# Kernel optimization log

Hardware: AMD Instinct MI355X
Metric: run time of the kernel (lower is better)

The kernel has to match this reference:

```python
import jax, jax.numpy as jnp
import numpy as np

S = 3000    # number of candidate spans (rows of g_i)
P = 80000   # total (mention, antecedent) pairs
GI = 768    # gi_dim
DD = 20     # distance/genre/speaker embedding dim
HID = 150   # mlp hidden dim (fixed in source)
ORDER = 2   # N: one higher-order refinement pass


def setup_inputs() -> dict:
    key = jax.random.key(0)
    ks = jax.random.split(key, 18)
    gij = 3 * GI + 3 * DD
    g_i = jax.random.normal(ks[0], (S, GI), jnp.float32)
    mention_scores = jax.random.normal(ks[1], (S, 1), jnp.float32)
    # sorted segment ids: ragged antecedent counts per mention, grouped contiguously
    mention_ids = jnp.sort(jax.random.randint(ks[2], (P,), 0, S, dtype=jnp.int32))
    antecedent_ids = jax.random.randint(ks[3], (P,), 0, S, dtype=jnp.int32)
    dist_bins = jax.random.randint(ks[4], (P,), 0, 10, dtype=jnp.int32)
    genre_ids = jax.random.randint(ks[5], (P,), 0, 7, dtype=jnp.int32) + 1   # 1..7, 0 is padding_idx
    speaker_ids = jax.random.randint(ks[6], (P,), 0, 2, dtype=jnp.int32) + 1  # 1..2, 0 is padding_idx
    w = lambda k, shp: 0.02 * jax.random.normal(k, shp, jnp.float32)
    dist_emb = w(ks[7], (10, DD))
    genre_emb = w(ks[8], (8, DD)).at[0].set(0.0)     # padding_idx=0
    speaker_emb = w(ks[9], (3, DD)).at[0].set(0.0)   # padding_idx=0
    W1 = w(ks[10], (gij, HID)); b1 = jnp.zeros((HID,), jnp.float32)
    W2 = w(ks[11], (HID, HID)); b2 = jnp.zeros((HID,), jnp.float32)
    W3 = w(ks[12], (HID, 1)); b3 = jnp.zeros((1,), jnp.float32)
    Wf = w(ks[13], (2 * GI, 1)); bf = jnp.zeros((1,), jnp.float32)
    return {"g_i": g_i, "mention_scores": mention_scores, "mention_ids": mention_ids,
            "antecedent_ids": antecedent_ids, "dist_bins": dist_bins, "genre_ids": genre_ids,
            "speaker_ids": speaker_ids, "dist_emb": dist_emb, "genre_emb": genre_emb,
            "speaker_emb": speaker_emb, "W1": W1, "b1": b1, "W2": W2, "b2": b2,
            "W3": W3, "b3": b3, "Wf": Wf, "bf": bf}


def _mlp(x, W1, b1, W2, b2, W3, b3):
    h = jax.nn.relu(x @ W1 + b1)
    h = jax.nn.relu(h @ W2 + b2)
    return h @ W3 + b3


def reference(g_i, mention_scores, mention_ids, antecedent_ids, dist_bins, genre_ids,
              speaker_ids, dist_emb, genre_emb, speaker_emb, W1, b1, W2, b2, W3, b3, Wf, bf):
    phi = jnp.concatenate([dist_emb[dist_bins], genre_emb[genre_ids], speaker_emb[speaker_ids]], axis=1)  # [P,60]
    seg = dict(num_segments=S, indices_are_sorted=True)
    g = g_i
    scores = None
    for n in range(ORDER):
        i_g = g[mention_ids]                # [P,GI] gather
        j_g = g[antecedent_ids]             # [P,GI] gather
        pairs = jnp.concatenate([i_g, j_g, i_g * j_g, phi], axis=1)  # [P,gij]
        scores = _mlp(pairs, W1, b1, W2, b2, W3, b3)                 # [P,1]
        if n < ORDER - 1:
            # higher_order_refinement: ragged segment softmax + weighted scatter update
            s = scores[:, 0]
            seg_max = jax.ops.segment_max(s, mention_ids, **seg)
            safe_max = jnp.where(jnp.isfinite(seg_max), seg_max, 0.0)
            e = jnp.exp(s - safe_max[mention_ids])
            denom = jax.ops.segment_sum(e, mention_ids, **seg)
            attn = e / jnp.where(denom > 0, denom, 1.0)[mention_ids]
            weighted = jax.ops.segment_sum(attn[:, None] * j_g, mention_ids, **seg)  # [S,GI]
            counts = jax.ops.segment_sum(jnp.ones_like(s), mention_ids, **seg)
            f = jax.nn.sigmoid(jnp.concatenate([g, weighted], axis=1) @ Wf + bf)  # [S,1]
            # NOTE: faithful to the source bug: f * mention_id (the integer index), not f * mention_g
            ids_f = jnp.arange(S, dtype=g.dtype)[:, None]
            g_new = f * ids_f + (1.0 - f) * weighted
            g = jnp.where(counts[:, None] > 0, g_new, g)
    s_i = mention_scores[mention_ids]
    s_j = mention_scores[antecedent_ids]
    coref_scores = s_i + s_j + scores       # [P,1]
    # segment softmax with an extra epsilon (score 0) logit per mention
    c = coref_scores[:, 0]
    seg_max = jax.ops.segment_max(c, mention_ids, **seg)
    m = jnp.maximum(jnp.where(jnp.isfinite(seg_max), seg_max, 0.0), 0.0)  # include epsilon logit 0
    e = jnp.exp(c - m[mention_ids])
    denom = jax.ops.segment_sum(e, mention_ids, **seg) + jnp.exp(-m)
    pair_probs = e / denom[mention_ids]     # [P]
    eps_probs = jnp.exp(-m) / denom         # [S]
    return coref_scores, pair_probs, eps_probs
```

## Files before the change

kernel.cpp:

```cpp
#include <hip/hip_runtime.h>

#define GI   768
#define HID  150
#define HPAD 160
#define DDIM 20

typedef __attribute__((ext_vector_type(8))) short v8s;
typedef __attribute__((ext_vector_type(16))) float f32x16;

#define MFMA(A, B, C) __builtin_amdgcn_mfma_f32_32x32x16_bf16(A, B, C, 0, 0, 0)

__device__ __forceinline__ ushort bf16rn(float x) {
  unsigned u = __float_as_uint(x);
  return (ushort)((u + 0x7fffu + ((u >> 16) & 1u)) >> 16);
}
__device__ __forceinline__ void bsplit(float x, ushort& h, ushort& l) {
  h = bf16rn(x);
  float fh = __uint_as_float((unsigned)h << 16);
  l = bf16rn(x - fh);
}
__device__ __forceinline__ void tsplit(float x, ushort& h, ushort& l) {
  unsigned u = __float_as_uint(x);
  h = (ushort)(u >> 16);
  float d = x - __uint_as_float(u & 0xffff0000u);
  l = (ushort)(__float_as_uint(d) >> 16);
}
__device__ __forceinline__ uint4 pack8(const ushort* v) {
  uint4 r;
  r.x = v[0] | ((unsigned)v[1] << 16); r.y = v[2] | ((unsigned)v[3] << 16);
  r.z = v[4] | ((unsigned)v[5] << 16); r.w = v[6] | ((unsigned)v[7] << 16);
  return r;
}
__device__ __forceinline__ v8s mk8(const ushort* v) {
  union { uint4 u; v8s s; } t;
  t.u = pack8(v);
  return t.s;
}

__device__ __forceinline__ int qoffb(int row, int kb) {
  return row * 96 + (kb ^ (((row >> 2) & 3) << 4));
}

__global__ void seg_kernel(const int* __restrict__ mI, int* __restrict__ segs,
                           int P, int S) {
  int m = blockIdx.x * 256 + threadIdx.x;
  if (m > S) return;
  int lo = 0, hi = P;
  while (lo < hi) { int mid = (lo + hi) >> 1; if (mI[mid] < m) lo = mid + 1; else hi = mid; }
  segs[m] = lo;
}

__global__ void phi_kernel(const float* __restrict__ de, const float* __restrict__ ge,
                           const float* __restrict__ se, const float* __restrict__ W1,
                           float* __restrict__ phiW) {
  int idx = blockIdx.x * 256 + threadIdx.x;
  if (idx >= 21 * HPAD) return;
  int row = idx / HPAD, h = idx % HPAD;
  float v = 0.f;
  if (h < HID) {
    const float* emb; int off;
    if (row < 10)      { emb = de + row * DDIM;        off = 0; }
    else if (row < 18) { emb = ge + (row - 10) * DDIM; off = DDIM; }
    else               { emb = se + (row - 18) * DDIM; off = 2 * DDIM; }
    for (int k = 0; k < DDIM; ++k) v += emb[k] * W1[(3 * GI + off + k) * HID + h];
  }
  phiW[row * HPAD + h] = v;
}

__global__ void pad2_kernel(const float* __restrict__ W1, const float* __restrict__ W2,
                            const float* __restrict__ b1, const float* __restrict__ b2,
                            const float* __restrict__ W3,
                            ushort* __restrict__ WThi, ushort* __restrict__ WTlo,
                            ushort* __restrict__ WBhi, ushort* __restrict__ WBlo,
                            ushort* __restrict__ W2Bhi, ushort* __restrict__ W2Blo,
                            float* __restrict__ b1p, float2* __restrict__ b2w3) {
  int idx = blockIdx.x * 256 + threadIdx.x;
  if (idx < 480 * GI) {
    int c = idx / GI, r = idx % GI;
    int seg = c / HPAD, h = c % HPAD;
    float x = (h < HID) ? W1[(size_t)(seg * GI + r) * HID + h] : 0.f;
    ushort hh, ll; bsplit(x, hh, ll);
    WThi[idx] = hh; WTlo[idx] = ll; return;
  }
  idx -= 480 * GI;
  if (idx < 5 * 48 * 512) {
    int c = idx / (48 * 512); int r1 = idx % (48 * 512);
    int s = r1 / 512; int r2 = r1 % 512;
    int l = r2 / 8, j = r2 % 8;
    int h = c * 32 + (l & 31);
    int k = s * 16 + 8 * (l >> 5) + j;
    float x = (h < HID) ? W1[(size_t)(2 * GI + k) * HID + h] : 0.f;
    ushort hh, ll; bsplit(x, hh, ll);
    WBhi[idx] = hh; WBlo[idx] = ll; return;
  }
  idx -= 5 * 48 * 512;
  if (idx < 5 * 10 * 512) {
    int rt = idx / (10 * 512); int r1 = idx % (10 * 512);
    int s = r1 / 512; int r2 = r1 % 512;
    int l = r2 / 8, j = r2 % 8;
    int h2 = rt * 32 + (l & 31);
    int k = s * 16 + 8 * (l >> 5) + j;
    float x = (k < HID && h2 < HID) ? W2[(size_t)k * HID + h2] : 0.f;
    ushort hh, ll; bsplit(x, hh, ll);
    W2Bhi[idx] = hh; W2Blo[idx] = ll; return;
  }
  idx -= 5 * 10 * 512;
  if (idx < HPAD) { b1p[idx] = (idx < HID) ? b1[idx] : 0.f; return; }
  idx -= HPAD;
  if (idx < HPAD) {
    b2w3[idx] = make_float2((idx < HID) ? b2[idx] : 0.f, (idx < HID) ? W3[idx] : 0.f);
    return;
  }
}

__global__ __launch_bounds__(320, 4) void pre2_kernel(
    const float* __restrict__ g, const ushort* __restrict__ WThi,
    const ushort* __restrict__ WTlo, float* __restrict__ pre, int S) {
  __shared__ char pool[24576];
  const int t = threadIdx.x;
  const int lane = t & 63, w = t >> 6;
  const int lcol = lane & 31, half = lane >> 5;
  const int row0 = blockIdx.x * 64;
  const int hb = blockIdx.y * HPAD;

  f32x16 acc0 = {}, acc1 = {};
  const ushort* wh = WThi + (size_t)(hb + w * 32 + lcol) * GI + 8 * half;
  const ushort* wl = WTlo + (size_t)(hb + w * 32 + lcol) * GI + 8 * half;

  const int qr = (t < 256) ? (t >> 2) : 0;
  const int qob = qoffb(qr, (t & 3) * 16);
  int srow = row0 + qr; if (srow >= S) srow = S - 1;
  const float* gp = g + (size_t)srow * GI + (t & 3) * 8;

  if (t < 256) {
    float4 a0 = *(const float4*)(gp), a1 = *(const float4*)(gp + 4);
    float xr[8] = {a0.x, a0.y, a0.z, a0.w, a1.x, a1.y, a1.z, a1.w};
    ushort hs[8], ls[8];
#pragma unroll
    for (int j = 0; j < 8; ++j) bsplit(xr[j], hs[j], ls[j]);
    *(uint4*)(pool + qob) = pack8(hs);
    *(uint4*)(pool + 6144 + qob) = pack8(ls);
  }
  v8s cwh0 = *(const v8s*)(wh), cwh1 = *(const v8s*)(wh + 16);
  v8s cwl0 = *(const v8s*)(wl), cwl1 = *(const v8s*)(wl + 16);
  __syncthreads();

  int cur = 0;
#pragma unroll 1
  for (int d0 = 0; d0 < GI; d0 += 32) {
    const bool has = (d0 + 32) < GI;
    const int dn = has ? d0 + 32 : 0;
    float4 na0, na1;
    if (t < 256) { na0 = *(const float4*)(gp + dn); na1 = *(const float4*)(gp + dn + 4); }
    v8s nwh0 = *(const v8s*)(wh + dn), nwh1 = *(const v8s*)(wh + dn + 16);
    v8s nwl0 = *(const v8s*)(wl + dn), nwl1 = *(const v8s*)(wl + dn + 16);

    const char* qh = pool + cur * 12288;
    const char* ql = qh + 6144;
    {
      const int kb = 16 * half;
      v8s a0h = *(const v8s*)(qh + qoffb(lcol, kb));
      v8s a0l = *(const v8s*)(ql + qoffb(lcol, kb));
      acc0 = MFMA(a0h, cwh0, acc0); acc0 = MFMA(a0l, cwh0, acc0); acc0 = MFMA(a0h, cwl0, acc0);
      v8s a1h = *(const v8s*)(qh + qoffb(32 + lcol, kb));
      v8s a1l = *(const v8s*)(ql + qoffb(32 + lcol, kb));
      acc1 = MFMA(a1h, cwh0, acc1); acc1 = MFMA(a1l, cwh0, acc1); acc1 = MFMA(a1h, cwl0, acc1);
    }
    {
      const int kb = 32 + 16 * half;
      v8s a0h = *(const v8s*)(qh + qoffb(lcol, kb));
      v8s a0l = *(const v8s*)(ql + qoffb(lcol, kb));
      acc0 = MFMA(a0h, cwh1, acc0); acc0 = MFMA(a0l, cwh1, acc0); acc0 = MFMA(a0h, cwl1, acc0);
      v8s a1h = *(const v8s*)(qh + qoffb(32 + lcol, kb));
      v8s a1l = *(const v8s*)(ql + qoffb(32 + lcol, kb));
      acc1 = MFMA(a1h, cwh1, acc1); acc1 = MFMA(a1l, cwh1, acc1); acc1 = MFMA(a1h, cwl1, acc1);
    }
    if (has && t < 256) {
      float xr[8] = {na0.x, na0.y, na0.z, na0.w, na1.x, na1.y, na1.z, na1.w};
      ushort hs[8], ls[8];
#pragma unroll
      for (int j = 0; j < 8; ++j) bsplit(xr[j], hs[j], ls[j]);
      char* dst = pool + (cur ^ 1) * 12288;
      *(uint4*)(dst + qob) = pack8(hs);
      *(uint4*)(dst + 6144 + qob) = pack8(ls);
    }
    cwh0 = nwh0; cwh1 = nwh1; cwl0 = nwl0; cwl1 = nwl1;
    __syncthreads();
    cur ^= 1;
  }

  const int h = w * 32 + lcol;
#pragma unroll
  for (int q = 0; q < 16; ++q) {
    int p = (q & 3) + 8 * (q >> 2) + 4 * half;
    int s0 = row0 + p;
    if (s0 < S) pre[(size_t)s0 * 320 + hb + h] = acc0[q];
    int s1 = row0 + 32 + p;
    if (s1 < S) pre[(size_t)s1 * 320 + hb + h] = acc1[q];
  }
}

__global__ __launch_bounds__(64, 3) void h1a_kernel(
    const float* __restrict__ g, const float* __restrict__ pre,
    const float* __restrict__ phiW,
    const ushort* __restrict__ WBhi, const ushort* __restrict__ WBlo,
    const float* __restrict__ b1p,
    const int* __restrict__ mI, const int* __restrict__ aI,
    const int* __restrict__ db, const int* __restrict__ ge, const int* __restrict__ sp,
    ushort* __restrict__ h1hi, ushort* __restrict__ h1lo, int P) {
  const int lane = threadIdx.x;
  const int lcol = lane & 31, half = lane >> 5;
  const int p0 = blockIdx.x * 32;

  const int myp = p0 + lcol;
  const int iA = mI[myp], jA = aI[myp];
  const int rdL = db[myp], rgL = 10 + ge[myp], rsL = 18 + sp[myp];

  const float* gi = g + (size_t)iA * GI + 8 * half;
  const float* gj = g + (size_t)jA * GI + 8 * half;

  f32x16 acc[5];
  {
    f32x16 z = {};
#pragma unroll
    for (int c = 0; c < 5; ++c) acc[c] = z;
  }

#pragma unroll 2
  for (int s = 0; s < 48; ++s) {
    const int d0 = s * 16;
    const float4 a0 = *(const float4*)(gi + d0);
    const float4 a1 = *(const float4*)(gi + d0 + 4);
    const float4 b0 = *(const float4*)(gj + d0);
    const float4 b1v = *(const float4*)(gj + d0 + 4);
    float xr[8] = {a0.x * b0.x, a0.y * b0.y, a0.z * b0.z, a0.w * b0.w,
                   a1.x * b1v.x, a1.y * b1v.y, a1.z * b1v.z, a1.w * b1v.w};
    ushort hs[8], ls[8];
#pragma unroll
    for (int j = 0; j < 8; ++j) tsplit(xr[j], hs[j], ls[j]);
    const v8s ah = mk8(hs), al = mk8(ls);
#pragma unroll
    for (int c = 0; c < 5; ++c) {
      const size_t o = ((size_t)(c * 48 + s) * 64 + lane) * 8;
      const v8s bh = *(const v8s*)(WBhi + o);
      const v8s bl = *(const v8s*)(WBlo + o);
      acc[c] = MFMA(ah, bh, acc[c]);
      acc[c] = MFMA(al, bh, acc[c]);
      acc[c] = MFMA(ah, bl, acc[c]);
    }
  }

#pragma unroll
  for (int q = 0; q < 16; ++q) {
    const int rr = (q & 3) + 8 * (q >> 2) + 4 * half;
    const int pI = __shfl(iA, rr);
    const int pJ = __shfl(jA, rr);
    const int rd = __shfl(rdL, rr), rg = __shfl(rgL, rr), rs = __shfl(rsL, rr);
    const float* preI = pre + (size_t)pI * 320;
    const float* preJ = pre + (size_t)pJ * 320 + 160;
    const size_t prow = (size_t)(p0 + rr) * 160;
#pragma unroll
    for (int c = 0; c < 5; ++c) {
      const int col = c * 32 + lcol;
      float v = acc[c][q] + b1p[col] + preI[col] + preJ[col]
              + phiW[rd * HPAD + col] + phiW[rg * HPAD + col] + phiW[rs * HPAD + col];
      v = fmaxf(v, 0.f);
      ushort hh, ll; tsplit(v, hh, ll);
      h1hi[prow + col] = hh;
      h1lo[prow + col] = ll;
    }
  }
}

__global__ __launch_bounds__(64, 3) void score3_kernel(
    const ushort* __restrict__ h1hi, const ushort* __restrict__ h1lo,
    const ushort* __restrict__ W2Bhi, const ushort* __restrict__ W2Blo,
    const float2* __restrict__ b2w3, const float* __restrict__ b3,
    float* __restrict__ sOut, int P) {
  const int lane = threadIdx.x;
  const int lcol = lane & 31, half = lane >> 5;
  const int p0 = blockIdx.x * 32;

  const ushort* hh = h1hi + (size_t)(p0 + lcol) * 160 + 8 * half;
  const ushort* hl = h1lo + (size_t)(p0 + lcol) * 160 + 8 * half;

  f32x16 acc[5];
  {
    f32x16 z = {};
#pragma unroll
    for (int r = 0; r < 5; ++r) acc[r] = z;
  }

#pragma unroll 2
  for (int s = 0; s < 10; ++s) {
    const v8s bh = *(const v8s*)(hh + s * 16);
    const v8s bl = *(const v8s*)(hl + s * 16);
#pragma unroll
    for (int r = 0; r < 5; ++r) {
      const size_t o = ((size_t)(r * 10 + s) * 64 + lane) * 8;
      const v8s ah = *(const v8s*)(W2Bhi + o);
      const v8s al = *(const v8s*)(W2Blo + o);
      acc[r] = MFMA(ah, bh, acc[r]);
      acc[r] = MFMA(al, bh, acc[r]);
      acc[r] = MFMA(ah, bl, acc[r]);
    }
  }

  float part = 0.f;
#pragma unroll
  for (int r = 0; r < 5; ++r) {
#pragma unroll
    for (int q = 0; q < 16; ++q) {
      const int h2 = r * 32 + (q & 3) + 8 * (q >> 2) + 4 * half;
      const float2 bw = b2w3[h2];
      part += fmaxf(acc[r][q] + bw.x, 0.f) * bw.y;
    }
  }
  part += __shfl_xor(part, 32);
  if (lane < 32) sOut[p0 + lane] = part + b3[0];
}

__global__ void mid_kernel(const float* __restrict__ g, const float* __restrict__ s1,
                           const int* __restrict__ segs, const int* __restrict__ aI,
                           const float* __restrict__ Wf, const float* __restrict__ bf,
                           float* __restrict__ g2) {
  const int m = blockIdx.x;
  const int t = threadIdx.x;
  const int st = segs[m], en = segs[m + 1], n = en - st;
  if (n == 0) {
    for (int d = t; d < GI; d += 256) g2[m * GI + d] = g[m * GI + d];
    return;
  }
  __shared__ float red[256];
  float mx = -INFINITY;
  for (int p = st + t; p < en; p += 256) mx = fmaxf(mx, s1[p]);
  red[t] = mx; __syncthreads();
  for (int s = 128; s > 0; s >>= 1) { if (t < s) red[t] = fmaxf(red[t], red[t + s]); __syncthreads(); }
  mx = red[0]; __syncthreads();
  float sm = 0.f;
  for (int p = st + t; p < en; p += 256) sm += expf(s1[p] - mx);
  red[t] = sm; __syncthreads();
  for (int s = 128; s > 0; s >>= 1) { if (t < s) red[t] += red[t + s]; __syncthreads(); }
  const float denom = red[0]; __syncthreads();
  float wv[3] = {0.f, 0.f, 0.f};
  for (int p = st; p < en; ++p) {
    float e = expf(s1[p] - mx);
    const float* gj = g + (size_t)aI[p] * GI;
#pragma unroll
    for (int u = 0; u < 3; ++u) wv[u] += e * gj[t + u * 256];
  }
#pragma unroll
  for (int u = 0; u < 3; ++u) wv[u] /= denom;
  float part = 0.f;
#pragma unroll
  for (int u = 0; u < 3; ++u) {
    int d = t + u * 256;
    part += g[m * GI + d] * Wf[d] + wv[u] * Wf[GI + d];
  }
  red[t] = part; __syncthreads();
  for (int s = 128; s > 0; s >>= 1) { if (t < s) red[t] += red[t + s]; __syncthreads(); }
  const float f = 1.f / (1.f + expf(-(red[0] + bf[0])));
#pragma unroll
  for (int u = 0; u < 3; ++u) {
    int d = t + u * 256;
    g2[m * GI + d] = f * (float)m + (1.f - f) * wv[u];
  }
}

__global__ void coref_kernel(const float* __restrict__ ms, const float* __restrict__ s2,
                             const int* __restrict__ mI, const int* __restrict__ aI,
                             float* __restrict__ out, int P) {
  int p = blockIdx.x * 256 + threadIdx.x;
  if (p >= P) return;
  out[p] = ms[mI[p]] + ms[aI[p]] + s2[p];
}

__global__ void final_kernel(const float* __restrict__ c, const int* __restrict__ segs,
                             float* __restrict__ pairP, float* __restrict__ epsP) {
  const int m = blockIdx.x;
  const int t = threadIdx.x;
  const int st = segs[m], en = segs[m + 1], n = en - st;
  __shared__ float red[256];
  float mx = -INFINITY;
  for (int p = st + t; p < en; p += 256) mx = fmaxf(mx, c[p]);
  red[t] = mx; __syncthreads();
  for (int s = 128; s > 0; s >>= 1) { if (t < s) red[t] = fmaxf(red[t], red[t + s]); __syncthreads(); }
  mx = red[0]; __syncthreads();
  const float m2 = (n > 0) ? fmaxf(mx, 0.f) : 0.f;
  float sm = 0.f;
  for (int p = st + t; p < en; p += 256) sm += expf(c[p] - m2);
  red[t] = sm; __syncthreads();
  for (int s = 128; s > 0; s >>= 1) { if (t < s) red[t] += red[t + s]; __syncthreads(); }
  const float denom = red[0] + expf(-m2);
  for (int p = st + t; p < en; p += 256) pairP[p] = expf(c[p] - m2) / denom;
  if (t == 0) epsP[m] = expf(-m2) / denom;
}

extern "C" void kernel_launch(void* const* d_in, const int* in_sizes, int n_in,
                              void* d_out, int out_size, void* d_ws, size_t ws_size,
                              hipStream_t stream) {
  const float* g_i  = (const float*)d_in[0];
  const float* ms   = (const float*)d_in[1];
  const int*   mI   = (const int*)d_in[2];
  const int*   aI   = (const int*)d_in[3];
  const int*   db   = (const int*)d_in[4];
  const int*   ge   = (const int*)d_in[5];
  const int*   sp   = (const int*)d_in[6];
  const float* de   = (const float*)d_in[7];
  const float* gemb = (const float*)d_in[8];
  const float* semb = (const float*)d_in[9];
  const float* W1   = (const float*)d_in[10];
  const float* b1   = (const float*)d_in[11];
  const float* W2   = (const float*)d_in[12];
  const float* b2   = (const float*)d_in[13];
  const float* W3   = (const float*)d_in[14];
  const float* b3   = (const float*)d_in[15];
  const float* Wf   = (const float*)d_in[16];
  const float* bf   = (const float*)d_in[17];

  const int S = in_sizes[0] / GI;
  const int P = in_sizes[2];
  float* out = (float*)d_out;

  char* ws = (char*)d_ws;
  size_t off = 0;
  auto take = [&](size_t bytes) -> char* {
    char* p = ws + off;
    off = (off + bytes + 15) & ~(size_t)15;
    return p;
  };
  int*    segs  = (int*)   take((size_t)(S + 1) * 4);
  float*  phiW  = (float*) take((size_t)21 * HPAD * 4);
  float*  pre   = (float*) take((size_t)S * 320 * 4);
  float*  g2    = (float*) take((size_t)S * GI * 4);
  float*  s1    = (float*) take((size_t)P * 4);
  float*  s2    = (float*) take((size_t)P * 4);
  ushort* WThi  = (ushort*)take((size_t)480 * GI * 2);
  ushort* WTlo  = (ushort*)take((size_t)480 * GI * 2);
  ushort* WBhi  = (ushort*)take((size_t)5 * 48 * 512 * 2);
  ushort* WBlo  = (ushort*)take((size_t)5 * 48 * 512 * 2);
  ushort* W2Bhi = (ushort*)take((size_t)5 * 10 * 512 * 2);
  ushort* W2Blo = (ushort*)take((size_t)5 * 10 * 512 * 2);
  float*  b1p   = (float*) take((size_t)HPAD * 4);
  float2* b2w3  = (float2*)take((size_t)HPAD * 8);
  ushort* h1hi  = (ushort*)take((size_t)P * 160 * 2);
  ushort* h1lo  = (ushort*)take((size_t)P * 160 * 2);

  const int gridSeg = (S + 1 + 255) / 256;
  const int gridPhi = (21 * HPAD + 255) / 256;
  const int padTot  = 480 * GI + 5 * 48 * 512 + 5 * 10 * 512 + 2 * HPAD;
  const int gridPad = (padTot + 255) / 256;
  const dim3 gridPre((S + 63) / 64, 2);
  const int gridH   = P / 32;
  const int gridCor = (P + 255) / 256;

  seg_kernel<<<gridSeg, 256, 0, stream>>>(mI, segs, P, S);
  phi_kernel<<<gridPhi, 256, 0, stream>>>(de, gemb, semb, W1, phiW);
  pad2_kernel<<<gridPad, 256, 0, stream>>>(W1, W2, b1, b2, W3, WThi, WTlo,
                                           WBhi, WBlo, W2Bhi, W2Blo, b1p, b2w3);

  pre2_kernel<<<gridPre, 320, 0, stream>>>(g_i, WThi, WTlo, pre, S);
  h1a_kernel<<<gridH, 64, 0, stream>>>(g_i, pre, phiW, WBhi, WBlo, b1p,
                                       mI, aI, db, ge, sp, h1hi, h1lo, P);
  score3_kernel<<<gridH, 64, 0, stream>>>(h1hi, h1lo, W2Bhi, W2Blo, b2w3, b3, s1, P);
  mid_kernel<<<S, 256, 0, stream>>>(g_i, s1, segs, aI, Wf, bf, g2);

  pre2_kernel<<<gridPre, 320, 0, stream>>>(g2, WThi, WTlo, pre, S);
  h1a_kernel<<<gridH, 64, 0, stream>>>(g2, pre, phiW, WBhi, WBlo, b1p,
                                       mI, aI, db, ge, sp, h1hi, h1lo, P);
  score3_kernel<<<gridH, 64, 0, stream>>>(h1hi, h1lo, W2Bhi, W2Blo, b2w3, b3, s2, P);

  coref_kernel<<<gridCor, 256, 0, stream>>>(ms, s2, mI, aI, out, P);
  final_kernel<<<S, 256, 0, stream>>>(out, segs, out + P, out + 2 * (size_t)P);
}
```

Before: 397.6 us.

## Replace pre2 GEMM with 16x16 MFMA kernel and prefetch weights in h1a

Replaces the shared-memory 64-row pre2 GEMM with a single-wavefront pre3 kernel that uses 16x16x32 bf16 MFMAs on weights pre-packed in the fragment layout, with one block per 16-column by 16-row tile. In h1a, the next step's g values and weight fragments are loaded into registers ahead of the MFMAs (software prefetch), and blocks are remapped so contiguous pair ranges sit on the same XCD. Launch bounds for h1a drop from 3 to 2 waves per unit to make room for the extra registers. The trade is reduced occupancy and a pre kernel with no LDS reuse of g across column tiles, so g is re-read from global once per column tile.

```diff
diff --git a/kernel.cpp b/kernel.cpp
--- a/kernel.cpp
+++ b/kernel.cpp
@@ -6,9 +6,11 @@
 #define DDIM 20
 
 typedef __attribute__((ext_vector_type(8))) short v8s;
+typedef __attribute__((ext_vector_type(4))) float f32x4;
 typedef __attribute__((ext_vector_type(16))) float f32x16;
 
-#define MFMA(A, B, C) __builtin_amdgcn_mfma_f32_32x32x16_bf16(A, B, C, 0, 0, 0)
+#define MFMA(A, B, C)   __builtin_amdgcn_mfma_f32_32x32x16_bf16(A, B, C, 0, 0, 0)
+#define MFMA16(A, B, C) __builtin_amdgcn_mfma_f32_16x16x32_bf16(A, B, C, 0, 0, 0)
 
 __device__ __forceinline__ ushort bf16rn(float x) {
   unsigned u = __float_as_uint(x);
@@ -35,10 +37,6 @@
   union { uint4 u; v8s s; } t;
   t.u = pack8(v);
   return t.s;
-}
-
-__device__ __forceinline__ int qoffb(int row, int kb) {
-  return row * 96 + (kb ^ (((row >> 2) & 3) << 4));
 }
 
 __global__ void seg_kernel(const int* __restrict__ mI, int* __restrict__ segs,
@@ -67,23 +65,18 @@
   phiW[row * HPAD + h] = v;
 }
 
+#define NWB  (5 * 48 * 512)
+#define NW16 (20 * 24 * 512)
+#define NW2B (5 * 10 * 512)
 __global__ void pad2_kernel(const float* __restrict__ W1, const float* __restrict__ W2,
                             const float* __restrict__ b1, const float* __restrict__ b2,
                             const float* __restrict__ W3,
-                            ushort* __restrict__ WThi, ushort* __restrict__ WTlo,
                             ushort* __restrict__ WBhi, ushort* __restrict__ WBlo,
+                            ushort* __restrict__ W16hi, ushort* __restrict__ W16lo,
                             ushort* __restrict__ W2Bhi, ushort* __restrict__ W2Blo,
                             float* __restrict__ b1p, float2* __restrict__ b2w3) {
   int idx = blockIdx.x * 256 + threadIdx.x;
-  if (idx < 480 * GI) {
-    int c = idx / GI, r = idx % GI;
-    int seg = c / HPAD, h = c % HPAD;
-    float x = (h < HID) ? W1[(size_t)(seg * GI + r) * HID + h] : 0.f;
-    ushort hh, ll; bsplit(x, hh, ll);
-    WThi[idx] = hh; WTlo[idx] = ll; return;
-  }
-  idx -= 480 * GI;
-  if (idx < 5 * 48 * 512) {
+  if (idx < NWB) {
     int c = idx / (48 * 512); int r1 = idx % (48 * 512);
     int s = r1 / 512; int r2 = r1 % 512;
     int l = r2 / 8, j = r2 % 8;
@@ -93,8 +86,20 @@
     ushort hh, ll; bsplit(x, hh, ll);
     WBhi[idx] = hh; WBlo[idx] = ll; return;
   }
-  idx -= 5 * 48 * 512;
-  if (idx < 5 * 10 * 512) {
+  idx -= NWB;
+  if (idx < NW16) {
+    int ct = idx / (24 * 512); int r1 = idx % (24 * 512);
+    int s = r1 / 512; int r2 = r1 % 512;
+    int l = r2 / 8, j = r2 % 8;
+    int col = ct * 16 + (l & 15);
+    int k = s * 32 + 8 * (l >> 4) + j;
+    int seg = col / HPAD, h = col % HPAD;
+    float x = (h < HID) ? W1[(size_t)(seg * GI + k) * HID + h] : 0.f;
+    ushort hh, ll; bsplit(x, hh, ll);
+    W16hi[idx] = hh; W16lo[idx] = ll; return;
+  }
+  idx -= NW16;
+  if (idx < NW2B) {
     int rt = idx / (10 * 512); int r1 = idx % (10 * 512);
     int s = r1 / 512; int r2 = r1 % 512;
     int l = r2 / 8, j = r2 % 8;
@@ -104,7 +109,7 @@
     ushort hh, ll; bsplit(x, hh, ll);
     W2Bhi[idx] = hh; W2Blo[idx] = ll; return;
   }
-  idx -= 5 * 10 * 512;
+  idx -= NW2B;
   if (idx < HPAD) { b1p[idx] = (idx < HID) ? b1[idx] : 0.f; return; }
   idx -= HPAD;
   if (idx < HPAD) {
@@ -113,94 +118,42 @@
   }
 }
 
-__global__ __launch_bounds__(320, 4) void pre2_kernel(
-    const float* __restrict__ g, const ushort* __restrict__ WThi,
-    const ushort* __restrict__ WTlo, float* __restrict__ pre, int S) {
-  __shared__ char pool[24576];
-  const int t = threadIdx.x;
-  const int lane = t & 63, w = t >> 6;
-  const int lcol = lane & 31, half = lane >> 5;
-  const int row0 = blockIdx.x * 64;
-  const int hb = blockIdx.y * HPAD;
-
-  f32x16 acc0 = {}, acc1 = {};
-  const ushort* wh = WThi + (size_t)(hb + w * 32 + lcol) * GI + 8 * half;
-  const ushort* wl = WTlo + (size_t)(hb + w * 32 + lcol) * GI + 8 * half;
-
-  const int qr = (t < 256) ? (t >> 2) : 0;
-  const int qob = qoffb(qr, (t & 3) * 16);
-  int srow = row0 + qr; if (srow >= S) srow = S - 1;
-  const float* gp = g + (size_t)srow * GI + (t & 3) * 8;
-
-  if (t < 256) {
-    float4 a0 = *(const float4*)(gp), a1 = *(const float4*)(gp + 4);
+__global__ __launch_bounds__(64, 4) void pre3_kernel(
+    const float* __restrict__ g, const ushort* __restrict__ W16hi,
+    const ushort* __restrict__ W16lo, float* __restrict__ pre, int S) {
+  const int lane = threadIdx.x;
+  const int ct = blockIdx.x;
+  const int row0 = blockIdx.y * 16;
+  int srow = row0 + (lane & 15); if (srow >= S) srow = S - 1;
+  const float* gp = g + (size_t)srow * GI + 8 * (lane >> 4);
+  const ushort* wph = W16hi + ((size_t)ct * 24 * 64 + lane) * 8;
+  const ushort* wpl = W16lo + ((size_t)ct * 24 * 64 + lane) * 8;
+
+  f32x4 acc = {};
+#pragma unroll 2
+  for (int s = 0; s < 24; ++s) {
+    const float4 a0 = *(const float4*)(gp + s * 32);
+    const float4 a1 = *(const float4*)(gp + s * 32 + 4);
+    const v8s bh = *(const v8s*)(wph + (size_t)s * 512);
+    const v8s bl = *(const v8s*)(wpl + (size_t)s * 512);
     float xr[8] = {a0.x, a0.y, a0.z, a0.w, a1.x, a1.y, a1.z, a1.w};
     ushort hs[8], ls[8];
 #pragma unroll
-    for (int j = 0; j < 8; ++j) bsplit(xr[j], hs[j], ls[j]);
-    *(uint4*)(pool + qob) = pack8(hs);
-    *(uint4*)(pool + 6144 + qob) = pack8(ls);
-  }
-  v8s cwh0 = *(const v8s*)(wh), cwh1 = *(const v8s*)(wh + 16);
-  v8s cwl0 = *(const v8s*)(wl), cwl1 = *(const v8s*)(wl + 16);
-  __syncthreads();
-
-  int cur = 0;
-#pragma unroll 1
-  for (int d0 = 0; d0 < GI; d0 += 32) {
-    const bool has = (d0 + 32) < GI;
-    const int dn = has ? d0 + 32 : 0;
-    float4 na0, na1;
-    if (t < 256) { na0 = *(const float4*)(gp + dn); na1 = *(const float4*)(gp + dn + 4); }
-    v8s nwh0 = *(const v8s*)(wh + dn), nwh1 = *(const v8s*)(wh + dn + 16);
-    v8s nwl0 = *(const v8s*)(wl + dn), nwl1 = *(const v8s*)(wl + dn + 16);
-
-    const char* qh = pool + cur * 12288;
-    const char* ql = qh + 6144;
-    {
-      const int kb = 16 * half;
-      v8s a0h = *(const v8s*)(qh + qoffb(lcol, kb));
-      v8s a0l = *(const v8s*)(ql + qoffb(lcol, kb));
-      acc0 = MFMA(a0h, cwh0, acc0); acc0 = MFMA(a0l, cwh0, acc0); acc0 = MFMA(a0h, cwl0, acc0);
-      v8s a1h = *(const v8s*)(qh + qoffb(32 + lcol, kb));
-      v8s a1l = *(const v8s*)(ql + qoffb(32 + lcol, kb));
-      acc1 = MFMA(a1h, cwh0, acc1); acc1 = MFMA(a1l, cwh0, acc1); acc1 = MFMA(a1h, cwl0, acc1);
-    }
-    {
-      const int kb = 32 + 16 * half;
-      v8s a0h = *(const v8s*)(qh + qoffb(lcol, kb));
-      v8s a0l = *(const v8s*)(ql + qoffb(lcol, kb));
-      acc0 = MFMA(a0h, cwh1, acc0); acc0 = MFMA(a0l, cwh1, acc0); acc0 = MFMA(a0h, cwl1, acc0);
-      v8s a1h = *(const v8s*)(qh + qoffb(32 + lcol, kb));
-      v8s a1l = *(const v8s*)(ql + qoffb(32 + lcol, kb));
-      acc1 = MFMA(a1h, cwh1, acc1); acc1 = MFMA(a1l, cwh1, acc1); acc1 = MFMA(a1h, cwl1, acc1);
-    }
-    if (has && t < 256) {
-      float xr[8] = {na0.x, na0.y, na0.z, na0.w, na1.x, na1.y, na1.z, na1.w};
-      ushort hs[8], ls[8];
-#pragma unroll
-      for (int j = 0; j < 8; ++j) bsplit(xr[j], hs[j], ls[j]);
-      char* dst = pool + (cur ^ 1) * 12288;
-      *(uint4*)(dst + qob) = pack8(hs);
-      *(uint4*)(dst + 6144 + qob) = pack8(ls);
-    }
-    cwh0 = nwh0; cwh1 = nwh1; cwl0 = nwl0; cwl1 = nwl1;
-    __syncthreads();
-    cur ^= 1;
-  }
-
-  const int h = w * 32 + lcol;
-#pragma unroll
-  for (int q = 0; q < 16; ++q) {
-    int p = (q & 3) + 8 * (q >> 2) + 4 * half;
-    int s0 = row0 + p;
-    if (s0 < S) pre[(size_t)s0 * 320 + hb + h] = acc0[q];
-    int s1 = row0 + 32 + p;
-    if (s1 < S) pre[(size_t)s1 * 320 + hb + h] = acc1[q];
-  }
-}
-
-__global__ __launch_bounds__(64, 3) void h1a_kernel(
+    for (int j = 0; j < 8; ++j) tsplit(xr[j], hs[j], ls[j]);
+    const v8s ah = mk8(hs), al = mk8(ls);
+    acc = MFMA16(ah, bh, acc);
+    acc = MFMA16(al, bh, acc);
+    acc = MFMA16(ah, bl, acc);
+  }
+  const int col = ct * 16 + (lane & 15);
+#pragma unroll
+  for (int r = 0; r < 4; ++r) {
+    int sr = row0 + (lane >> 4) * 4 + r;
+    if (sr < S) pre[(size_t)sr * 320 + col] = acc[r];
+  }
+}
+
+__global__ __launch_bounds__(64, 2) void h1a_kernel(
     const float* __restrict__ g, const float* __restrict__ pre,
     const float* __restrict__ phiW,
     const ushort* __restrict__ WBhi, const ushort* __restrict__ WBlo,
@@ -210,7 +163,13 @@
     ushort* __restrict__ h1hi, ushort* __restrict__ h1lo, int P) {
   const int lane = threadIdx.x;
   const int lcol = lane & 31, half = lane >> 5;
-  const int p0 = blockIdx.x * 32;
+
+  const int nwg = gridDim.x;
+  const int orig = blockIdx.x;
+  const int xcd = orig & 7, idx8 = orig >> 3;
+  const int qq = nwg >> 3, rr = nwg & 7;
+  const int wg = (xcd < rr ? xcd * (qq + 1) : rr * (qq + 1) + (xcd - rr) * qq) + idx8;
+  const int p0 = wg * 32;
 
   const int myp = p0 + lcol;
   const int iA = mI[myp], jA = aI[myp];
@@ -226,39 +185,59 @@
     for (int c = 0; c < 5; ++c) acc[c] = z;
   }
 
+  float4 A0 = *(const float4*)(gi);
+  float4 A1 = *(const float4*)(gi + 4);
+  float4 B0 = *(const float4*)(gj);
+  float4 B1 = *(const float4*)(gj + 4);
+  v8s wh[5], wl[5];
+#pragma unroll
+  for (int c = 0; c < 5; ++c) {
+    const size_t o = ((size_t)(c * 48) * 64 + lane) * 8;
+    wh[c] = *(const v8s*)(WBhi + o);
+    wl[c] = *(const v8s*)(WBlo + o);
+  }
+
 #pragma unroll 2
   for (int s = 0; s < 48; ++s) {
-    const int d0 = s * 16;
-    const float4 a0 = *(const float4*)(gi + d0);
-    const float4 a1 = *(const float4*)(gi + d0 + 4);
-    const float4 b0 = *(const float4*)(gj + d0);
-    const float4 b1v = *(const float4*)(gj + d0 + 4);
-    float xr[8] = {a0.x * b0.x, a0.y * b0.y, a0.z * b0.z, a0.w * b0.w,
-                   a1.x * b1v.x, a1.y * b1v.y, a1.z * b1v.z, a1.w * b1v.w};
+    const int sn = (s < 47) ? s + 1 : 47;
+    const int dn = sn * 16;
+    const float4 nA0 = *(const float4*)(gi + dn);
+    const float4 nA1 = *(const float4*)(gi + dn + 4);
+    const float4 nB0 = *(const float4*)(gj + dn);
+    const float4 nB1 = *(const float4*)(gj + dn + 4);
+    v8s nwh[5], nwl[5];
+#pragma unroll
+    for (int c = 0; c < 5; ++c) {
+      const size_t o = ((size_t)(c * 48 + sn) * 64 + lane) * 8;
+      nwh[c] = *(const v8s*)(WBhi + o);
+      nwl[c] = *(const v8s*)(WBlo + o);
+    }
+    float xr[8] = {A0.x * B0.x, A0.y * B0.y, A0.z * B0.z, A0.w * B0.w,
+                   A1.x * B1.x, A1.y * B1.y, A1.z * B1.z, A1.w * B1.w};
     ushort hs[8], ls[8];
 #pragma unroll
     for (int j = 0; j < 8; ++j) tsplit(xr[j], hs[j], ls[j]);
     const v8s ah = mk8(hs), al = mk8(ls);
 #pragma unroll
     for (int c = 0; c < 5; ++c) {
-      const size_t o = ((size_t)(c * 48 + s) * 64 + lane) * 8;
-      const v8s bh = *(const v8s*)(WBhi + o);
-      const v8s bl = *(const v8s*)(WBlo + o);
-      acc[c] = MFMA(ah, bh, acc[c]);
-      acc[c] = MFMA(al, bh, acc[c]);
-      acc[c] = MFMA(ah, bl, acc[c]);
+      acc[c] = MFMA(ah, wh[c], acc[c]);
+      acc[c] = MFMA(al, wh[c], acc[c]);
+      acc[c] = MFMA(ah, wl[c], acc[c]);
     }
+    A0 = nA0; A1 = nA1; B0 = nB0; B1 = nB1;
+#pragma unroll
+    for (int c = 0; c < 5; ++c) { wh[c] = nwh[c]; wl[c] = nwl[c]; }
   }
 
 #pragma unroll
   for (int q = 0; q < 16; ++q) {
-    const int rr = (q & 3) + 8 * (q >> 2) + 4 * half;
-    const int pI = __shfl(iA, rr);
-    const int pJ = __shfl(jA, rr);
-    const int rd = __shfl(rdL, rr), rg = __shfl(rgL, rr), rs = __shfl(rsL, rr);
+    const int rr2 = (q & 3) + 8 * (q >> 2) + 4 * half;
+    const int pI = __shfl(iA, rr2);
+    const int pJ = __shfl(jA, rr2);
+    const int rd = __shfl(rdL, rr2), rg = __shfl(rgL, rr2), rs = __shfl(rsL, rr2);
     const float* preI = pre + (size_t)pI * 320;
     const float* preJ = pre + (size_t)pJ * 320 + 160;
-    const size_t prow = (size_t)(p0 + rr) * 160;
+    const size_t prow = (size_t)(p0 + rr2) * 160;
 #pragma unroll
     for (int c = 0; c < 5; ++c) {
       const int col = c * 32 + lcol;
@@ -435,12 +414,12 @@
   float*  g2    = (float*) take((size_t)S * GI * 4);
   float*  s1    = (float*) take((size_t)P * 4);
   float*  s2    = (float*) take((size_t)P * 4);
-  ushort* WThi  = (ushort*)take((size_t)480 * GI * 2);
-  ushort* WTlo  = (ushort*)take((size_t)480 * GI * 2);
-  ushort* WBhi  = (ushort*)take((size_t)5 * 48 * 512 * 2);
-  ushort* WBlo  = (ushort*)take((size_t)5 * 48 * 512 * 2);
-  ushort* W2Bhi = (ushort*)take((size_t)5 * 10 * 512 * 2);
-  ushort* W2Blo = (ushort*)take((size_t)5 * 10 * 512 * 2);
+  ushort* WBhi  = (ushort*)take((size_t)NWB * 2);
+  ushort* WBlo  = (ushort*)take((size_t)NWB * 2);
+  ushort* W16hi = (ushort*)take((size_t)NW16 * 2);
+  ushort* W16lo = (ushort*)take((size_t)NW16 * 2);
+  ushort* W2Bhi = (ushort*)take((size_t)NW2B * 2);
+  ushort* W2Blo = (ushort*)take((size_t)NW2B * 2);
   float*  b1p   = (float*) take((size_t)HPAD * 4);
   float2* b2w3  = (float2*)take((size_t)HPAD * 8);
   ushort* h1hi  = (ushort*)take((size_t)P * 160 * 2);
@@ -448,24 +427,24 @@
 
   const int gridSeg = (S + 1 + 255) / 256;
   const int gridPhi = (21 * HPAD + 255) / 256;
-  const int padTot  = 480 * GI + 5 * 48 * 512 + 5 * 10 * 512 + 2 * HPAD;
+  const int padTot  = NWB + NW16 + NW2B + 2 * HPAD;
   const int gridPad = (padTot + 255) / 256;
-  const dim3 gridPre((S + 63) / 64, 2);
+  const dim3 gridPre(20, (S + 15) / 16);
   const int gridH   = P / 32;
   const int gridCor = (P + 255) / 256;
 
   seg_kernel<<<gridSeg, 256, 0, stream>>>(mI, segs, P, S);
   phi_kernel<<<gridPhi, 256, 0, stream>>>(de, gemb, semb, W1, phiW);
-  pad2_kernel<<<gridPad, 256, 0, stream>>>(W1, W2, b1, b2, W3, WThi, WTlo,
-                                           WBhi, WBlo, W2Bhi, W2Blo, b1p, b2w3);
-
-  pre2_kernel<<<gridPre, 320, 0, stream>>>(g_i, WThi, WTlo, pre, S);
+  pad2_kernel<<<gridPad, 256, 0, stream>>>(W1, W2, b1, b2, W3, WBhi, WBlo,
+                                           W16hi, W16lo, W2Bhi, W2Blo, b1p, b2w3);
+
+  pre3_kernel<<<gridPre, 64, 0, stream>>>(g_i, W16hi, W16lo, pre, S);
   h1a_kernel<<<gridH, 64, 0, stream>>>(g_i, pre, phiW, WBhi, WBlo, b1p,
                                        mI, aI, db, ge, sp, h1hi, h1lo, P);
   score3_kernel<<<gridH, 64, 0, stream>>>(h1hi, h1lo, W2Bhi, W2Blo, b2w3, b3, s1, P);
   mid_kernel<<<S, 256, 0, stream>>>(g_i, s1, segs, aI, Wf, bf, g2);
 
-  pre2_kernel<<<gridPre, 320, 0, stream>>>(g2, WThi, WTlo, pre, S);
+  pre3_kernel<<<gridPre, 64, 0, stream>>>(g2, W16hi, W16lo, pre, S);
   h1a_kernel<<<gridH, 64, 0, stream>>>(g2, pre, phiW, WBhi, WBlo, b1p,
                                        mI, aI, db, ge, sp, h1hi, h1lo, P);
   score3_kernel<<<gridH, 64, 0, stream>>>(h1hi, h1lo, W2Bhi, W2Blo, b2w3, b3, s2, P);
```

Result: slower. 495.6 us (+24.7%).
